# Optimization experiments

Hardware: AMD Instinct MI355X
Metric: run time of the kernel (lower is better)

The kernel has to match this reference:

```python
import jax, jax.numpy as jnp
import numpy as np

H, D = 8, 16          # heads, head_dim
HID = H * D           # hidden_channels = 128
OUT = 64              # out_channels
N = 25_000            # nodes per node type (author, paper)
E = 250_000           # edges per relation
L = 2                 # num HGT layers
T = 2                 # node types
R = 2                 # edge types: (author->paper), (paper->author)
SCALE = 1.0 / np.sqrt(HID).astype(np.float32)


def setup_inputs() -> dict:
    key = jax.random.key(0)
    ks = jax.random.split(key, 16)
    f = lambda k, s: jax.random.normal(k, s, dtype=jnp.float32)
    return dict(
        x_author=f(ks[0], (N, HID)),
        x_paper=f(ks[1], (N, HID)),
        edge_writes=jax.random.randint(ks[2], (2, E), 0, N, dtype=jnp.int32),
        edge_rev=jax.random.randint(ks[3], (2, E), 0, N, dtype=jnp.int32),
        W_in=f(ks[4], (T, HID, HID)) * SCALE,
        b_in=jnp.zeros((T, HID), jnp.float32),
        Wq=f(ks[5], (L, T, HID, HID)) * SCALE,
        bq=jnp.zeros((L, T, HID), jnp.float32),
        Wk=f(ks[6], (L, T, HID, HID)) * SCALE,
        bk=jnp.zeros((L, T, HID), jnp.float32),
        Wv=f(ks[7], (L, T, HID, HID)) * SCALE,
        bv=jnp.zeros((L, T, HID), jnp.float32),
        Wa=f(ks[8], (L, T, HID, HID)) * SCALE,
        ba=jnp.zeros((L, T, HID), jnp.float32),
        skip=jnp.ones((L, T), jnp.float32),
        a_rel=f(ks[9], (L, R, H, D, D)) * (1.0 / np.sqrt(D).astype(np.float32)),
        m_rel=f(ks[10], (L, R, H, D, D)) * (1.0 / np.sqrt(D).astype(np.float32)),
        p_rel=jnp.ones((L, R, H), jnp.float32),
        W_out=f(ks[11], (HID, OUT)) * SCALE,
        b_out=jnp.zeros((OUT,), jnp.float32),
    )


def _seg_softmax(scores, seg, n):
    # scores [E, H]; softmax over edges sharing the same destination node.
    m = jax.ops.segment_max(scores, seg, num_segments=n)
    e = jnp.exp(scores - m[seg])
    s = jax.ops.segment_sum(e, seg, num_segments=n)
    return e / (s[seg] + 1e-16)


def _hnn_forward(x_author, x_paper, edge_writes, edge_rev, W_in, b_in, Wq, bq,
                 Wk, bk, Wv, bv, Wa, ba, skip, a_rel, m_rel, p_rel, W_out, b_out):
    # input projection per node type + relu
    xs = [jax.nn.relu(x_author @ W_in[0] + b_in[0]),
          jax.nn.relu(x_paper @ W_in[1] + b_in[1])]
    edges = [(0, 1, edge_writes), (1, 0, edge_rev)]  # (src_type, dst_type, edge_index)
    inv_sqrt_d = jnp.float32(1.0 / np.sqrt(D))
    for l in range(L):
        q = [(xs[t] @ Wq[l, t] + bq[l, t]).reshape(N, H, D) for t in range(T)]
        k = [(xs[t] @ Wk[l, t] + bk[l, t]).reshape(N, H, D) for t in range(T)]
        v = [(xs[t] @ Wv[l, t] + bv[l, t]).reshape(N, H, D) for t in range(T)]
        agg = [jnp.zeros((N, HID), xs[0].dtype) for _ in range(T)]
        for r, (s, t, ei) in enumerate(edges):
            src, dst = ei[0], ei[1]
            # per-relation transform of gathered keys/values: [E,H,D] x [H,D,D]
            k_e = jnp.einsum('ehd,hdf->ehf', k[s][src], a_rel[l, r])
            score = jnp.sum(q[t][dst] * k_e, axis=-1) * p_rel[l, r] * inv_sqrt_d  # [E,H]
            alpha = _seg_softmax(score, dst, N)
            v_e = jnp.einsum('ehd,hdf->ehf', v[s][src], m_rel[l, r])
            msg = (v_e * alpha[:, :, None]).reshape(E, HID)
            agg[t] = agg[t] + jax.ops.segment_sum(msg, dst, num_segments=N)
        new_xs = []
        for t in range(T):
            out = jax.nn.gelu(agg[t], approximate=False) @ Wa[l, t] + ba[l, t]
            beta = jax.nn.sigmoid(skip[l, t])
            new_xs.append(beta * out + (1.0 - beta) * xs[t])  # gated residual (in==out dims)
        xs = new_xs
    return (xs[0] @ W_out + b_out, xs[1] @ W_out + b_out)


def reference(x_author, x_paper, edge_writes, edge_rev, W_in, b_in, Wq, bq, Wk,
              bk, Wv, bv, Wa, ba, skip, a_rel, m_rel, p_rel, W_out, b_out):
    return _hnn_forward(x_author, x_paper, edge_writes, edge_rev, W_in, b_in,
                        Wq, bq, Wk, bk, Wv, bv, Wa, ba, skip, a_rel, m_rel,
                        p_rel, W_out, b_out)
```

## Files before the change

### kernel.cpp

```cpp
#include <hip/hip_runtime.h>
#include <math.h>

#define N_NODES 25000
#define E_EDGES 250000
#define HID 128
#define OUTC 64
#define NPB 98

using bf16x8 = __attribute__((ext_vector_type(8))) short;
using f32x4  = __attribute__((ext_vector_type(4))) float;

__device__ __forceinline__ unsigned short f2bf(float f) {
    unsigned u = __float_as_uint(f);
    u = (u + 0x7fffu + ((u >> 16) & 1u)) >> 16;
    return (unsigned short)u;
}
__device__ __forceinline__ float bf2f(unsigned short h) {
    return __uint_as_float(((unsigned)h) << 16);
}
__device__ __forceinline__ float gelu_f(float x) {
    return 0.5f * x * (1.0f + erff(x * 0.70710678118654752440f));
}

__global__ void hist2(const int* __restrict__ e0, const int* __restrict__ e1,
                      int* __restrict__ cnt) {
    int r = blockIdx.y;
    const int* d = (r ? e1 : e0) + E_EDGES;
    int e = blockIdx.x * 256 + threadIdx.x;
    if (e < E_EDGES) atomicAdd(&cnt[r * N_NODES + d[e]], 1);
}

__global__ void csr_partial(const int* __restrict__ cnt, int* __restrict__ part) {
    int r = blockIdx.y, b = blockIdx.x, t = threadIdx.x;
    int idx = b * 256 + t;
    int v = (idx < N_NODES) ? cnt[r * N_NODES + idx] : 0;
    #pragma unroll
    for (int d = 1; d < 64; d <<= 1) v += __shfl_xor(v, d);
    __shared__ int ws[4];
    if ((t & 63) == 0) ws[t >> 6] = v;
    __syncthreads();
    if (t == 0) part[r * NPB + b] = ws[0] + ws[1] + ws[2] + ws[3];
}

__global__ void csr_scanpart(int* __restrict__ part) {
    int w = threadIdx.x >> 6, lane = threadIdx.x & 63;
    int base = w * NPB;
    int a = part[base + lane];
    int b = (lane < NPB - 64) ? part[base + 64 + lane] : 0;
    int va = a, vb = b;
    #pragma unroll
    for (int d = 1; d < 64; d <<= 1) { int u = __shfl_up(va, d); if (lane >= d) va += u; }
    #pragma unroll
    for (int d = 1; d < 64; d <<= 1) { int u = __shfl_up(vb, d); if (lane >= d) vb += u; }
    int tot0 = __shfl(va, 63);
    part[base + lane] = va - a;
    if (lane < NPB - 64) part[base + 64 + lane] = vb - b + tot0;
}

__global__ void csr_write(int* __restrict__ cnt, const int* __restrict__ part,
                          int* __restrict__ rowptr) {
    int r = blockIdx.y, b = blockIdx.x, t = threadIdx.x;
    int idx = b * 256 + t;
    int v = (idx < N_NODES) ? cnt[r * N_NODES + idx] : 0;
    int lane = t & 63, w = t >> 6;
    int iv = v;
    #pragma unroll
    for (int d = 1; d < 64; d <<= 1) { int u = __shfl_up(iv, d); if (lane >= d) iv += u; }
    __shared__ int wtot[4];
    if (lane == 63) wtot[w] = iv;
    __syncthreads();
    int woff = part[r * NPB + b];
    #pragma unroll
    for (int i = 0; i < 4; i++) if (i < w) woff += wtot[i];
    int excl = woff + iv - v;
    if (idx < N_NODES) {
        rowptr[r * (N_NODES + 1) + idx] = excl;
        cnt[r * N_NODES + idx] = excl;
    }
    if (b == 0 && t == 0) rowptr[r * (N_NODES + 1) + N_NODES] = E_EDGES;
}

__global__ void scatter2(const int* __restrict__ e0, const int* __restrict__ e1,
                         int* __restrict__ cursor, int* __restrict__ srcs) {
    int r = blockIdx.y;
    const int* e = r ? e1 : e0;
    int i = blockIdx.x * 256 + threadIdx.x;
    if (i < E_EDGES) {
        int p = atomicAdd(&cursor[r * N_NODES + e[E_EDGES + i]], 1);
        srcs[r * E_EDGES + p] = e[i];
    }
}

__global__ void tconv(const float* __restrict__ src, unsigned short* __restrict__ dst, int C) {
    int m = blockIdx.y;
    int idx = blockIdx.x * 256 + threadIdx.x;
    if (idx >= C * 128) return;
    int c = idx >> 7, k = idx & 127;
    dst[(size_t)m * C * 128 + idx] = f2bf(src[(size_t)m * 128 * C + k * C + c]);
}

__global__ __launch_bounds__(256) void prep_qkv(
    const float* __restrict__ Wq, const float* __restrict__ bq,
    const float* __restrict__ Wk, const float* __restrict__ bk,
    const float* __restrict__ Wv, const float* __restrict__ bv,
    const float* __restrict__ a_rel, const float* __restrict__ m_rel,
    unsigned short* __restrict__ WT, float* __restrict__ bfq)
{
    int p = blockIdx.y;
    __shared__ float sA[2048], sM[2048];
    for (int i = threadIdx.x; i < 2048; i += 256) {
        sA[i] = a_rel[p * 2048 + i];
        sM[i] = m_rel[p * 2048 + i];
    }
    __syncthreads();
    int idx = blockIdx.x * 256 + threadIdx.x;
    if (idx >= 384 * 129) return;
    int c = idx / 129;
    int ik = idx - c * 129;
    const float* wq = Wq + (size_t)p * 16384;
    const float* wk = Wk + (size_t)p * 16384;
    const float* wv = Wv + (size_t)p * 16384;
    float val;
    if (c < 128) {
        val = (ik < 128) ? wq[ik * 128 + c] : bq[p * 128 + c];
    } else if (c < 256) {
        int cc = c - 128, h = cc >> 4, f = cc & 15;
        const float* row = (ik < 128) ? &wk[ik * 128 + h * 16] : &bk[p * 128 + h * 16];
        float s = 0.f;
        #pragma unroll
        for (int d = 0; d < 16; d++) s = fmaf(row[d], sA[h * 256 + d * 16 + f], s);
        val = s;
    } else {
        int cc = c - 256, h = cc >> 4, f = cc & 15;
        const float* row = (ik < 128) ? &wv[ik * 128 + h * 16] : &bv[p * 128 + h * 16];
        float s = 0.f;
        #pragma unroll
        for (int d = 0; d < 16; d++) s = fmaf(row[d], sM[h * 256 + d * 16 + f], s);
        val = s;
    }
    if (ik < 128) WT[(size_t)p * 384 * 128 + (size_t)c * 128 + ik] = f2bf(val);
    else bfq[p * 384 + c] = val;
}

template<int NOUT, int BN, int OUTMODE, int A_FP32>
__global__ __launch_bounds__(256) void mm4_kernel(
    const void* __restrict__ A0, const void* __restrict__ A1,
    const unsigned short* __restrict__ W0, const unsigned short* __restrict__ W1,
    const float* __restrict__ b0, const float* __restrict__ b1,
    const unsigned short* __restrict__ res0, const unsigned short* __restrict__ res1,
    const float* __restrict__ skipp,
    void* __restrict__ C0, void* __restrict__ C1, int nrows)
{
    constexpr int CF = BN / 16;
    __shared__ unsigned short sW[BN * 128];
    int z = blockIdx.z;
    const void* Av = z ? A1 : A0;
    const unsigned short* W = z ? W1 : W0;
    const float* bias = z ? b1 : b0;
    const unsigned short* res = z ? res1 : res0;
    void* Cv = z ? C1 : C0;

    int t = threadIdx.x;
    int w = t >> 6, lane = t & 63, lo = lane & 15, hi = lane >> 4;
    int col0 = blockIdx.y * BN;
    int rowbase = blockIdx.x * 128 + w * 32;

    const unsigned short* Wg = W + (size_t)col0 * 128;
    #pragma unroll
    for (int it = 0; it < BN / 16; ++it) {
        int idx = it * 256 + t;
        int col = idx >> 4, ch = idx & 15;
        bf16x8 v = *(const bf16x8*)(Wg + (size_t)col * 128 + ch * 8);
        *(bf16x8*)&sW[col * 128 + ((ch ^ (col & 7)) << 3)] = v;
    }

    bf16x8 a[2][4];
    #pragma unroll
    for (int rf = 0; rf < 2; rf++) {
        int r = rowbase + rf * 16 + lo;
        if (r > nrows - 1) r = nrows - 1;
        if (A_FP32) {
            const float* Arow = (const float*)Av + (size_t)r * HID;
            #pragma unroll
            for (int kk = 0; kk < 4; kk++) {
                float4 x0 = *(const float4*)(Arow + kk * 32 + hi * 8);
                float4 x1 = *(const float4*)(Arow + kk * 32 + hi * 8 + 4);
                bf16x8 v;
                v[0] = (short)f2bf(x0.x); v[1] = (short)f2bf(x0.y);
                v[2] = (short)f2bf(x0.z); v[3] = (short)f2bf(x0.w);
                v[4] = (short)f2bf(x1.x); v[5] = (short)f2bf(x1.y);
                v[6] = (short)f2bf(x1.z); v[7] = (short)f2bf(x1.w);
                a[rf][kk] = v;
            }
        } else {
            const unsigned short* Arow = (const unsigned short*)Av + (size_t)r * HID;
            #pragma unroll
            for (int kk = 0; kk < 4; kk++)
                a[rf][kk] = *(const bf16x8*)(Arow + kk * 32 + hi * 8);
        }
    }
    __syncthreads();

    f32x4 acc[2][CF];
    #pragma unroll
    for (int rf = 0; rf < 2; rf++)
        #pragma unroll
        for (int cf = 0; cf < CF; cf++) acc[rf][cf] = (f32x4){0.f, 0.f, 0.f, 0.f};

    #pragma unroll
    for (int cf = 0; cf < CF; cf++) {
        int colb = cf * 16 + lo;
        int sbase = colb * 128;
        int sx = colb & 7;
        bf16x8 bfr[4];
        #pragma unroll
        for (int kk = 0; kk < 4; kk++) {
            int ch = kk * 4 + hi;
            bfr[kk] = *(const bf16x8*)&sW[sbase + ((ch ^ sx) << 3)];
        }
        #pragma unroll
        for (int kk = 0; kk < 4; kk++) {
            acc[0][cf] = __builtin_amdgcn_mfma_f32_16x16x32_bf16(a[0][kk], bfr[kk], acc[0][cf], 0, 0, 0);
            acc[1][cf] = __builtin_amdgcn_mfma_f32_16x16x32_bf16(a[1][kk], bfr[kk], acc[1][cf], 0, 0, 0);
        }
    }

    float beta = 0.f, omb = 0.f;
    if (OUTMODE == 2) { float sv = skipp[z]; beta = 1.f / (1.f + __expf(-sv)); omb = 1.f - beta; }
    #pragma unroll
    for (int rf = 0; rf < 2; rf++) {
        #pragma unroll
        for (int cf = 0; cf < CF; cf++) {
            int col = col0 + cf * 16 + lo;
            float bb = bias[col];
            #pragma unroll
            for (int j = 0; j < 4; j++) {
                int r = rowbase + rf * 16 + hi * 4 + j;
                if (r >= nrows) continue;
                float v = acc[rf][cf][j] + bb;
                if (OUTMODE == 1) v = fmaxf(v, 0.f);
                if (OUTMODE == 2) v = beta * v + omb * bf2f(res[(size_t)r * NOUT + col]);
                if (OUTMODE == 3) ((float*)Cv)[(size_t)r * NOUT + col] = v;
                else ((unsigned short*)Cv)[(size_t)r * NOUT + col] = f2bf(v);
            }
        }
    }
}

__global__ __launch_bounds__(256) void attn3_kernel(
    const unsigned short* __restrict__ qkv0, const unsigned short* __restrict__ qkv1,
    const int* __restrict__ rowptr, const int* __restrict__ srcs,
    const float* __restrict__ prel,
    unsigned short* __restrict__ agg0, unsigned short* __restrict__ agg1, int n)
{
    int r = blockIdx.y;
    const unsigned short* qd = r ? qkv0 : qkv1;
    const unsigned short* sv = r ? qkv1 : qkv0;
    unsigned short* agg      = r ? agg0 : agg1;
    const int* rp = rowptr + r * (N_NODES + 1);
    const int* ss = srcs + r * E_EDGES;

    int gid = blockIdx.x * 256 + threadIdx.x;
    int nid = gid >> 5, lane = gid & 31;
    if (nid >= n) return;
    int c0 = lane << 2;
    int h = lane >> 2;
    const unsigned short* qrow = qd + (size_t)nid * 384 + c0;
    float q0 = bf2f(qrow[0]), q1 = bf2f(qrow[1]), q2 = bf2f(qrow[2]), q3 = bf2f(qrow[3]);
    float p = prel[r * 8 + h] * 0.25f;
    float m = -INFINITY, ssum = 0.f;
    float ax = 0.f, ay = 0.f, az = 0.f, aw = 0.f;
    int beg = rp[nid], end = rp[nid + 1];
    if (beg < end) {
        int s0 = ss[beg];
        const unsigned short* srow0 = sv + (size_t)s0 * 384;
        ushort4 kv = *(const ushort4*)(srow0 + 128 + c0);
        ushort4 vv = *(const ushort4*)(srow0 + 256 + c0);
        for (int i = beg; i < end; i++) {
            int inx = i + 1 < end ? i + 1 : end - 1;
            int sn = ss[inx];
            const unsigned short* srn = sv + (size_t)sn * 384;
            ushort4 kvn = *(const ushort4*)(srn + 128 + c0);
            ushort4 vvn = *(const ushort4*)(srn + 256 + c0);
            float part = q0 * bf2f(kv.x) + q1 * bf2f(kv.y) + q2 * bf2f(kv.z) + q3 * bf2f(kv.w);
            part += __shfl_xor(part, 1);
            part += __shfl_xor(part, 2);
            float score = part * p;
            float nm = fmaxf(m, score);
            float resc = __expf(m - nm);
            float e = __expf(score - nm);
            ssum = ssum * resc + e;
            ax = ax * resc + e * bf2f(vv.x);
            ay = ay * resc + e * bf2f(vv.y);
            az = az * resc + e * bf2f(vv.z);
            aw = aw * resc + e * bf2f(vv.w);
            m = nm;
            kv = kvn; vv = vvn;
        }
    }
    float inv = 1.f / (ssum + 1e-16f);
    ushort4 o;
    o.x = f2bf(gelu_f(ax * inv)); o.y = f2bf(gelu_f(ay * inv));
    o.z = f2bf(gelu_f(az * inv)); o.w = f2bf(gelu_f(aw * inv));
    *(ushort4*)(agg + (size_t)nid * HID + c0) = o;
}

extern "C" void kernel_launch(void* const* d_in, const int* in_sizes, int n_in,
                              void* d_out, int out_size, void* d_ws, size_t ws_size,
                              hipStream_t stream)
{
    (void)in_sizes; (void)n_in; (void)out_size; (void)ws_size;
    const float* x_author = (const float*)d_in[0];
    const float* x_paper  = (const float*)d_in[1];
    const int*   e_writes = (const int*)d_in[2];
    const int*   e_rev    = (const int*)d_in[3];
    const float* W_in = (const float*)d_in[4];
    const float* b_in = (const float*)d_in[5];
    const float* Wq = (const float*)d_in[6];
    const float* bq = (const float*)d_in[7];
    const float* Wk = (const float*)d_in[8];
    const float* bk = (const float*)d_in[9];
    const float* Wv = (const float*)d_in[10];
    const float* bv = (const float*)d_in[11];
    const float* Wa = (const float*)d_in[12];
    const float* ba = (const float*)d_in[13];
    const float* skip = (const float*)d_in[14];
    const float* a_rel = (const float*)d_in[15];
    const float* m_rel = (const float*)d_in[16];
    const float* p_rel = (const float*)d_in[17];
    const float* W_out = (const float*)d_in[18];
    const float* b_out = (const float*)d_in[19];
    float* out = (float*)d_out;

    const size_t NC = (size_t)N_NODES * HID;
    const size_t NQ = (size_t)N_NODES * 384;
    unsigned short* U = (unsigned short*)d_ws;
    unsigned short* cur0 = U;             unsigned short* cur1 = U + NC;
    unsigned short* agg0 = U + 2 * NC;    unsigned short* agg1 = U + 3 * NC;
    unsigned short* qkv0 = U + 4 * NC;    unsigned short* qkv1 = U + 4 * NC + NQ;
    unsigned short* WTin  = U + 4 * NC + 2 * NQ;
    unsigned short* WTqkv = WTin + 2 * 16384;
    unsigned short* WTa   = WTqkv + 4 * 49152;
    unsigned short* WTout = WTa + 4 * 16384;
    float* bfq = (float*)(WTout + OUTC * 128);
    int* I      = (int*)(bfq + 4 * 384);
    int* cnt    = I;
    int* part   = I + 2 * N_NODES;
    int* rowptr = part + 2 * NPB;
    int* srcs   = rowptr + 2 * (N_NODES + 1);

    dim3 blk(256);
    int eGrid = (E_EDGES + 255) / 256;
    int mmX = (N_NODES + 127) / 128;
    int attnX = (N_NODES * 32 + 255) / 256;
    int prepX = (384 * 129 + 255) / 256;

    hipMemsetAsync(cnt, 0, 2 * N_NODES * sizeof(int), stream);
    hist2<<<dim3(eGrid, 2), blk, 0, stream>>>(e_writes, e_rev, cnt);
    csr_partial<<<dim3(NPB, 2), blk, 0, stream>>>(cnt, part);
    csr_scanpart<<<1, 128, 0, stream>>>(part);
    csr_write<<<dim3(NPB, 2), blk, 0, stream>>>(cnt, part, rowptr);
    scatter2<<<dim3(eGrid, 2), blk, 0, stream>>>(e_writes, e_rev, cnt, srcs);

    tconv<<<dim3(64, 2), blk, 0, stream>>>(W_in, WTin, HID);
    tconv<<<dim3(64, 4), blk, 0, stream>>>(Wa, WTa, HID);
    tconv<<<dim3(32, 1), blk, 0, stream>>>(W_out, WTout, OUTC);
    prep_qkv<<<dim3(prepX, 4), blk, 0, stream>>>(Wq, bq, Wk, bk, Wv, bv, a_rel, m_rel, WTqkv, bfq);

    mm4_kernel<HID, 128, 1, 1><<<dim3(mmX, 1, 2), blk, 0, stream>>>(
        x_author, x_paper, WTin, WTin + 16384, b_in, b_in + HID,
        nullptr, nullptr, nullptr, cur0, cur1, N_NODES);

    for (int l = 0; l < 2; l++) {
        mm4_kernel<384, 128, 0, 0><<<dim3(mmX, 3, 2), blk, 0, stream>>>(
            cur0, cur1,
            WTqkv + (size_t)(l * 2 + 0) * 49152, WTqkv + (size_t)(l * 2 + 1) * 49152,
            bfq + (l * 2 + 0) * 384, bfq + (l * 2 + 1) * 384,
            nullptr, nullptr, nullptr, qkv0, qkv1, N_NODES);
        attn3_kernel<<<dim3(attnX, 2), blk, 0, stream>>>(
            qkv0, qkv1, rowptr, srcs, p_rel + (size_t)l * 16, agg0, agg1, N_NODES);
        mm4_kernel<HID, 128, 2, 0><<<dim3(mmX, 1, 2), blk, 0, stream>>>(
            agg0, agg1,
            WTa + (size_t)(l * 2 + 0) * 16384, WTa + (size_t)(l * 2 + 1) * 16384,
            ba + (l * 2 + 0) * HID, ba + (l * 2 + 1) * HID,
            cur0, cur1, skip + l * 2, cur0, cur1, N_NODES);
    }

    mm4_kernel<OUTC, 64, 3, 0><<<dim3(mmX, 1, 2), blk, 0, stream>>>(
        cur0, cur1, WTout, WTout, b_out, b_out,
        nullptr, nullptr, nullptr, out, out + (size_t)N_NODES * OUTC, N_NODES);
}
```

Before: 392.4 us.

## Interleave K/V columns and split each node's edges across two half-wavefronts

The QKV projection now writes K and V interleaved in groups of four, so each lane fetches its K and V slice with a single 16-byte load instead of two 8-byte loads. The attention kernel gives each destination node a full 64-lane wavefront: the two halves process alternating edges with their own online softmax, then merge running max, sum and accumulators with cross-half shuffles. This is meant to cut gather transactions and double memory-level parallelism per node. The cost is an extra merge step, idle lanes on low-degree nodes, and only half the lanes writing output.

```diff
diff --git a/kernel.cpp b/kernel.cpp
--- a/kernel.cpp
+++ b/kernel.cpp
@@ -8,6 +8,7 @@
 #define NPB 98
 
 using bf16x8 = __attribute__((ext_vector_type(8))) short;
+using u16x8  = __attribute__((ext_vector_type(8))) unsigned short;
 using f32x4  = __attribute__((ext_vector_type(4))) float;
 
 __device__ __forceinline__ unsigned short f2bf(float f) {
@@ -142,7 +143,7 @@
     else bfq[p * 384 + c] = val;
 }
 
-template<int NOUT, int BN, int OUTMODE, int A_FP32>
+template<int NOUT, int BN, int OUTMODE, int A_FP32, int KVIL>
 __global__ __launch_bounds__(256) void mm4_kernel(
     const void* __restrict__ A0, const void* __restrict__ A1,
     const unsigned short* __restrict__ W0, const unsigned short* __restrict__ W1,
@@ -233,6 +234,11 @@
         for (int cf = 0; cf < CF; cf++) {
             int col = col0 + cf * 16 + lo;
             float bb = bias[col];
+            int scol = col;
+            if (KVIL) {
+                if (col >= 256)      { int cc = col - 256; scol = 128 + ((cc >> 2) << 3) + 4 + (cc & 3); }
+                else if (col >= 128) { int cc = col - 128; scol = 128 + ((cc >> 2) << 3) + (cc & 3); }
+            }
             #pragma unroll
             for (int j = 0; j < 4; j++) {
                 int r = rowbase + rf * 16 + hi * 4 + j;
@@ -241,13 +247,13 @@
                 if (OUTMODE == 1) v = fmaxf(v, 0.f);
                 if (OUTMODE == 2) v = beta * v + omb * bf2f(res[(size_t)r * NOUT + col]);
                 if (OUTMODE == 3) ((float*)Cv)[(size_t)r * NOUT + col] = v;
-                else ((unsigned short*)Cv)[(size_t)r * NOUT + col] = f2bf(v);
+                else ((unsigned short*)Cv)[(size_t)r * NOUT + scol] = f2bf(v);
             }
         }
     }
 }
 
-__global__ __launch_bounds__(256) void attn3_kernel(
+__global__ __launch_bounds__(256) void attn4_kernel(
     const unsigned short* __restrict__ qkv0, const unsigned short* __restrict__ qkv1,
     const int* __restrict__ rowptr, const int* __restrict__ srcs,
     const float* __restrict__ prel,
@@ -260,49 +266,60 @@
     const int* rp = rowptr + r * (N_NODES + 1);
     const int* ss = srcs + r * E_EDGES;
 
-    int gid = blockIdx.x * 256 + threadIdx.x;
-    int nid = gid >> 5, lane = gid & 31;
+    int nid = blockIdx.x * 4 + (threadIdx.x >> 6);
     if (nid >= n) return;
-    int c0 = lane << 2;
-    int h = lane >> 2;
+    int lane = threadIdx.x & 63;
+    int half = lane >> 5;
+    int g = lane & 31;
+    int c0 = g << 2;
+    int h = g >> 2;
+
     const unsigned short* qrow = qd + (size_t)nid * 384 + c0;
     float q0 = bf2f(qrow[0]), q1 = bf2f(qrow[1]), q2 = bf2f(qrow[2]), q3 = bf2f(qrow[3]);
     float p = prel[r * 8 + h] * 0.25f;
-    float m = -INFINITY, ssum = 0.f;
+
+    float m = -1e30f, ssum = 0.f;
     float ax = 0.f, ay = 0.f, az = 0.f, aw = 0.f;
     int beg = rp[nid], end = rp[nid + 1];
-    if (beg < end) {
-        int s0 = ss[beg];
-        const unsigned short* srow0 = sv + (size_t)s0 * 384;
-        ushort4 kv = *(const ushort4*)(srow0 + 128 + c0);
-        ushort4 vv = *(const ushort4*)(srow0 + 256 + c0);
-        for (int i = beg; i < end; i++) {
-            int inx = i + 1 < end ? i + 1 : end - 1;
-            int sn = ss[inx];
-            const unsigned short* srn = sv + (size_t)sn * 384;
-            ushort4 kvn = *(const ushort4*)(srn + 128 + c0);
-            ushort4 vvn = *(const ushort4*)(srn + 256 + c0);
-            float part = q0 * bf2f(kv.x) + q1 * bf2f(kv.y) + q2 * bf2f(kv.z) + q3 * bf2f(kv.w);
-            part += __shfl_xor(part, 1);
-            part += __shfl_xor(part, 2);
-            float score = part * p;
+    int i0 = beg + half;
+    if (i0 < end) {
+        u16x8 kv = *(const u16x8*)(sv + (size_t)ss[i0] * 384 + 128 + (g << 3));
+        for (int i = i0; i < end; i += 2) {
+            int nx = i + 2 < end ? i + 2 : i;
+            u16x8 kvn = *(const u16x8*)(sv + (size_t)ss[nx] * 384 + 128 + (g << 3));
+            float sc = q0 * bf2f(kv[0]) + q1 * bf2f(kv[1]) + q2 * bf2f(kv[2]) + q3 * bf2f(kv[3]);
+            sc += __shfl_xor(sc, 1);
+            sc += __shfl_xor(sc, 2);
+            float score = sc * p;
             float nm = fmaxf(m, score);
             float resc = __expf(m - nm);
             float e = __expf(score - nm);
             ssum = ssum * resc + e;
-            ax = ax * resc + e * bf2f(vv.x);
-            ay = ay * resc + e * bf2f(vv.y);
-            az = az * resc + e * bf2f(vv.z);
-            aw = aw * resc + e * bf2f(vv.w);
+            ax = ax * resc + e * bf2f(kv[4]);
+            ay = ay * resc + e * bf2f(kv[5]);
+            az = az * resc + e * bf2f(kv[6]);
+            aw = aw * resc + e * bf2f(kv[7]);
             m = nm;
-            kv = kvn; vv = vvn;
+            kv = kvn;
         }
     }
-    float inv = 1.f / (ssum + 1e-16f);
-    ushort4 o;
-    o.x = f2bf(gelu_f(ax * inv)); o.y = f2bf(gelu_f(ay * inv));
-    o.z = f2bf(gelu_f(az * inv)); o.w = f2bf(gelu_f(aw * inv));
-    *(ushort4*)(agg + (size_t)nid * HID + c0) = o;
+    float mo = __shfl_xor(m, 32);
+    float nm2 = fmaxf(m, mo);
+    float f = __expf(m - nm2);
+    ssum *= f; ax *= f; ay *= f; az *= f; aw *= f;
+    ssum += __shfl_xor(ssum, 32);
+    ax += __shfl_xor(ax, 32);
+    ay += __shfl_xor(ay, 32);
+    az += __shfl_xor(az, 32);
+    aw += __shfl_xor(aw, 32);
+
+    if (half == 0) {
+        float inv = 1.f / (ssum + 1e-16f);
+        ushort4 o;
+        o.x = f2bf(gelu_f(ax * inv)); o.y = f2bf(gelu_f(ay * inv));
+        o.z = f2bf(gelu_f(az * inv)); o.w = f2bf(gelu_f(aw * inv));
+        *(ushort4*)(agg + (size_t)nid * HID + c0) = o;
+    }
 }
 
 extern "C" void kernel_launch(void* const* d_in, const int* in_sizes, int n_in,
@@ -352,7 +369,7 @@
     dim3 blk(256);
     int eGrid = (E_EDGES + 255) / 256;
     int mmX = (N_NODES + 127) / 128;
-    int attnX = (N_NODES * 32 + 255) / 256;
+    int attnX = (N_NODES + 3) / 4;
     int prepX = (384 * 129 + 255) / 256;
 
     hipMemsetAsync(cnt, 0, 2 * N_NODES * sizeof(int), stream);
@@ -367,26 +384,26 @@
     tconv<<<dim3(32, 1), blk, 0, stream>>>(W_out, WTout, OUTC);
     prep_qkv<<<dim3(prepX, 4), blk, 0, stream>>>(Wq, bq, Wk, bk, Wv, bv, a_rel, m_rel, WTqkv, bfq);
 
-    mm4_kernel<HID, 128, 1, 1><<<dim3(mmX, 1, 2), blk, 0, stream>>>(
+    mm4_kernel<HID, 128, 1, 1, 0><<<dim3(mmX, 1, 2), blk, 0, stream>>>(
         x_author, x_paper, WTin, WTin + 16384, b_in, b_in + HID,
         nullptr, nullptr, nullptr, cur0, cur1, N_NODES);
 
     for (int l = 0; l < 2; l++) {
-        mm4_kernel<384, 128, 0, 0><<<dim3(mmX, 3, 2), blk, 0, stream>>>(
+        mm4_kernel<384, 128, 0, 0, 1><<<dim3(mmX, 3, 2), blk, 0, stream>>>(
             cur0, cur1,
             WTqkv + (size_t)(l * 2 + 0) * 49152, WTqkv + (size_t)(l * 2 + 1) * 49152,
             bfq + (l * 2 + 0) * 384, bfq + (l * 2 + 1) * 384,
             nullptr, nullptr, nullptr, qkv0, qkv1, N_NODES);
-        attn3_kernel<<<dim3(attnX, 2), blk, 0, stream>>>(
+        attn4_kernel<<<dim3(attnX, 2), blk, 0, stream>>>(
             qkv0, qkv1, rowptr, srcs, p_rel + (size_t)l * 16, agg0, agg1, N_NODES);
-        mm4_kernel<HID, 128, 2, 0><<<dim3(mmX, 1, 2), blk, 0, stream>>>(
+        mm4_kernel<HID, 128, 2, 0, 0><<<dim3(mmX, 1, 2), blk, 0, stream>>>(
             agg0, agg1,
             WTa + (size_t)(l * 2 + 0) * 16384, WTa + (size_t)(l * 2 + 1) * 16384,
             ba + (l * 2 + 0) * HID, ba + (l * 2 + 1) * HID,
             cur0, cur1, skip + l * 2, cur0, cur1, N_NODES);
     }
 
-    mm4_kernel<OUTC, 64, 3, 0><<<dim3(mmX, 1, 2), blk, 0, stream>>>(
+    mm4_kernel<OUTC, 64, 3, 0, 0><<<dim3(mmX, 1, 2), blk, 0, stream>>>(
         cur0, cur1, WTout, WTout, b_out, b_out,
         nullptr, nullptr, nullptr, out, out + (size_t)N_NODES * OUTC, N_NODES);
 }
```

New measurement: 395.7 us. Within noise of the previous version (+0.8%).
